# Performance work log

Hardware: AMD Instinct MI355X
Metric: run time of the kernel (lower is better)

## Reference

```python
import jax, jax.numpy as jnp
import numpy as np

T = 2048        # q_len (current chunk)
P = 2048        # past KV cache length
HID = 4096      # hidden_size
H = 32          # num_attention_heads
D = HID // H    # head_dim = 128
THETA = 10000.0


def apply_rope(x, pos):
    # x: [H, T, D], pos: [T] int
    half = D // 2
    inv_freq = 1.0 / (THETA ** (jnp.arange(0, half, dtype=jnp.float32) / half))
    ang = pos.astype(jnp.float32)[:, None] * inv_freq[None, :]      # [T, D/2]
    cos = jnp.concatenate([jnp.cos(ang), jnp.cos(ang)], axis=-1)[None]  # [1, T, D]
    sin = jnp.concatenate([jnp.sin(ang), jnp.sin(ang)], axis=-1)[None]
    rot = jnp.concatenate([-x[..., half:], x[..., :half]], axis=-1)
    return x * cos + rot * sin


def setup_inputs() -> dict:
    key = jax.random.key(0)
    ks = jax.random.split(key, 8)
    s = 1.0 / np.sqrt(HID)
    inp = {
        "hidden_states": jax.random.normal(ks[0], (T, HID), dtype=jnp.float32),
        "attention_mask": jnp.triu(jnp.full((T, T), -jnp.inf, dtype=jnp.float32), k=1),
        "Wq": jax.random.normal(ks[1], (HID, HID), dtype=jnp.float32) * s,
        "Wk": jax.random.normal(ks[2], (HID, HID), dtype=jnp.float32) * s,
        "Wv": jax.random.normal(ks[3], (HID, HID), dtype=jnp.float32) * s,
        "Wo": jax.random.normal(ks[4], (HID, HID), dtype=jnp.float32) * s,
        "past_k": jax.random.normal(ks[5], (H, P, D), dtype=jnp.float32),
        "past_v": jax.random.normal(ks[6], (H, P, D), dtype=jnp.float32),
        "position_ids": P + jnp.arange(T, dtype=jnp.int32),
        "past_length": P,
    }
    return inp


def reference(hidden_states, attention_mask, Wq, Wk, Wv, Wo, past_k, past_v,
              position_ids, past_length):
    # QKV projections -> [H, T, D]
    proj = lambda W: (hidden_states @ W).reshape(T, H, D).transpose(1, 0, 2)
    q, k, v = proj(Wq), proj(Wk), proj(Wv)
    q = apply_rope(q, position_ids)
    k = apply_rope(k, position_ids)

    scale = 1.0 / jnp.sqrt(jnp.float32(D))
    # scores against past cache and current chunk (fp32 softmax, as in source)
    past_dots = (jnp.einsum('htd,hsd->hts', q, past_k) * scale).astype(jnp.float32)
    pmask = jnp.where(jnp.arange(P) < past_length, 0.0, -jnp.inf)  # [P]
    past_dots = past_dots + pmask
    cur = ((jnp.einsum('htd,hsd->hts', q, k) * scale) + attention_mask).astype(jnp.float32)

    # online-softmax merge via logsumexp combination
    past_lse = jax.scipy.special.logsumexp(past_dots, axis=-1, keepdims=True)
    cur_lse = jax.scipy.special.logsumexp(cur, axis=-1, keepdims=True)
    tot_lse = jnp.logaddexp(past_lse, cur_lse)
    pw = jnp.exp(past_dots - tot_lse).astype(q.dtype)
    cw = jnp.exp(cur - tot_lse).astype(q.dtype)

    out = jnp.einsum('hts,hsd->htd', pw, past_v) + jnp.einsum('hts,hsd->htd', cw, v)
    out = jnp.where(past_length == 0,
                    jnp.einsum('hts,hsd->htd', jax.nn.softmax(cur, axis=-1).astype(q.dtype), v),
                    out)
    out = out.transpose(1, 0, 2).reshape(T, HID)   # [T, hidden]
    return out @ Wo
```

## Files before the change

kernel.cpp:

```cpp
#include <hip/hip_runtime.h>
#include <cstdint>
#include <cstddef>

#define T_LEN 2048
#define PAST_MAX 2048
#define HID 4096
#define NHEAD 32
#define DHEAD 128

typedef __bf16 bf16_t;
typedef __bf16 bf16x4 __attribute__((ext_vector_type(4)));
typedef __bf16 bf16x8 __attribute__((ext_vector_type(8)));
typedef float  f32x4  __attribute__((ext_vector_type(4)));
typedef float  f32x16 __attribute__((ext_vector_type(16)));
typedef unsigned int u32x4 __attribute__((ext_vector_type(4)));

__device__ __forceinline__ void gload16(const void* g, void* l){
  __builtin_amdgcn_global_load_lds((const __attribute__((address_space(1))) void*)g,
                                   (__attribute__((address_space(3))) void*)l,
                                   16, 0, 0);
}

__device__ __forceinline__ unsigned pack_bf16(float a, float b){
  const unsigned ua = __builtin_bit_cast(unsigned short, (bf16_t)a);
  const unsigned ub = __builtin_bit_cast(unsigned short, (bf16_t)b);
  return ua | (ub << 16);
}

__global__ void cvt2_k(const float* __restrict__ a, bf16_t* __restrict__ ao,
                       const float* __restrict__ b, bf16_t* __restrict__ bo, int n4){
  int i = blockIdx.x * 256 + threadIdx.x;
  if (i < n4){
    const float4 v = ((const float4*)a)[i];
    bf16x4 o = { (bf16_t)v.x, (bf16_t)v.y, (bf16_t)v.z, (bf16_t)v.w };
    ((bf16x4*)ao)[i] = o;
  } else {
    i -= n4;
    const float4 v = ((const float4*)b)[i];
    bf16x4 o = { (bf16_t)v.x, (bf16_t)v.y, (bf16_t)v.z, (bf16_t)v.w };
    ((bf16x4*)bo)[i] = o;
  }
}

__global__ __launch_bounds__(256) void transpose2_k(const float* __restrict__ in,
                                                    bf16_t* __restrict__ out, int R, int C){
  __shared__ float tile[64][65];
  const int r0 = blockIdx.x << 6, c0 = blockIdx.y << 6;
  const size_t bo = (size_t)blockIdx.z * (size_t)R * (size_t)C;
  const int tx = threadIdx.x & 15, ty = threadIdx.x >> 4;
#pragma unroll
  for (int k = 0; k < 4; ++k){
    const float4 v = *(const float4*)(in + bo + (size_t)(r0 + ty + 16*k) * C + c0 + tx*4);
    float* tp = &tile[ty + 16*k][tx*4];
    tp[0] = v.x; tp[1] = v.y; tp[2] = v.z; tp[3] = v.w;
  }
  __syncthreads();
  const int rr0 = (threadIdx.x & 7) * 8;
  const int ccb = threadIdx.x >> 3;
#pragma unroll
  for (int k = 0; k < 2; ++k){
    const int cc = ccb + 32*k;
    bf16x8 o;
#pragma unroll
    for (int j = 0; j < 8; ++j) o[j] = (bf16_t)tile[rr0 + j][cc];
    *(bf16x8*)(out + bo + (size_t)(c0 + cc) * R + r0 + rr0) = o;
  }
}

__global__ __launch_bounds__(256) void transpose3_k(
    const float* __restrict__ s0, const float* __restrict__ s1, const float* __restrict__ s2,
    bf16_t* __restrict__ d0, bf16_t* __restrict__ d1, bf16_t* __restrict__ d2){
  __shared__ float tile[64][65];
  const float* in = (blockIdx.z == 0) ? s0 : (blockIdx.z == 1) ? s1 : s2;
  bf16_t* out = (blockIdx.z == 0) ? d0 : (blockIdx.z == 1) ? d1 : d2;
  const int r0 = blockIdx.x << 6, c0 = blockIdx.y << 6;
  const int tx = threadIdx.x & 15, ty = threadIdx.x >> 4;
#pragma unroll
  for (int k = 0; k < 4; ++k){
    const float4 v = *(const float4*)(in + (size_t)(r0 + ty + 16*k) * HID + c0 + tx*4);
    float* tp = &tile[ty + 16*k][tx*4];
    tp[0] = v.x; tp[1] = v.y; tp[2] = v.z; tp[3] = v.w;
  }
  __syncthreads();
  const int rr0 = (threadIdx.x & 7) * 8;
  const int ccb = threadIdx.x >> 3;
#pragma unroll
  for (int k = 0; k < 2; ++k){
    const int cc = ccb + 32*k;
    bf16x8 o;
#pragma unroll
    for (int j = 0; j < 8; ++j) o[j] = (bf16_t)tile[rr0 + j][cc];
    *(bf16x8*)(out + (size_t)(c0 + cc) * HID + r0 + rr0) = o;
  }
}

__global__ void ropek_k(bf16_t* __restrict__ K, const int* __restrict__ pos){
  const int idx = blockIdx.x * 256 + threadIdx.x;
  const int i = idx & 63;
  const int t = (idx >> 6) & (T_LEN - 1);
  const int h = idx >> 17;
  const size_t base = ((size_t)h * T_LEN + t) * DHEAD;
  const float p = (float)pos[t];
  const float inv = __expf(-(float)i * 0.14391156605212898f);
  const float ang = p * inv;
  float sn, cs;
  sincosf(ang, &sn, &cs);
  const float b0 = (float)K[base + i], b1 = (float)K[base + i + 64];
  K[base + i]      = (bf16_t)(b0 * cs - b1 * sn);
  K[base + i + 64] = (bf16_t)(b1 * cs + b0 * sn);
}

__global__ __launch_bounds__(512, 1) void gemmqkv4p_k(
    const bf16_t* __restrict__ A,
    const bf16_t* __restrict__ B0, const bf16_t* __restrict__ B1, const bf16_t* __restrict__ B2,
    bf16_t* __restrict__ OQ, bf16_t* __restrict__ OK2, bf16_t* __restrict__ OVT, int cpx)
{
  const int bid = blockIdx.x;
  const int wg  = (bid & 7) * cpx + (bid >> 3);
  const int mt  = wg & 7;
  const int rest = wg >> 3;
  const int z   = rest >> 5;
  const int nt  = rest & 31;
  const int m0  = mt << 8;
  const int n0  = nt << 7;
  const bf16_t* __restrict__ B = (z == 0) ? B0 : (z == 1) ? B1 : B2;

  const int tid = threadIdx.x;
  const int wv = tid >> 6, lane = tid & 63, lm = lane & 15, g = lane >> 4;
  const int wr = wv >> 1, wc = wv & 1;

  __shared__ __align__(16) char smem[98304];

  const f32x4 fzero = {0.f, 0.f, 0.f, 0.f};
  f32x4 acc[4][4];
#pragma unroll
  for (int i = 0; i < 4; ++i)
#pragma unroll
    for (int j = 0; j < 4; ++j) acc[i][j] = fzero;

  int srow[2], schk[2];
#pragma unroll
  for (int i = 0; i < 2; ++i){
    const int c = i * 512 + tid;
    srow[i] = c >> 3;
    schk[i] = (c & 7) ^ (srow[i] & 7);
  }
  const int sdst0 = ((0 * 512 + wv * 64) << 4);
  const int sdst1 = ((1 * 512 + wv * 64) << 4);

  auto stg = [&](int kt, int op){
    if (kt < 64){
      char* dst = smem + (kt & 1) * 49152 + op * 16384;
      const bf16_t* base = (op < 2) ? A + (size_t)(m0 + (op << 7)) * HID
                                    : B + (size_t)n0 * HID;
      base += kt * 64;
      gload16(base + (size_t)srow[0] * HID + schk[0] * 8, dst + sdst0);
      gload16(base + (size_t)srow[1] * HID + schk[1] * 8, dst + sdst1);
    }
  };

  const int koff0 = ((g)     ^ (lm & 7)) << 4;
  const int koff1 = ((4 + g) ^ (lm & 7)) << 4;
  const int abase = ((wr >> 1) << 14) + ((((wr & 1) << 6) + lm) << 7);
  const int bbase = 32768 + ((((wc << 6)) + lm) << 7);

  bf16x8 bfr[4][2];
  auto dsB = [&](int buf){
    const char* p = smem + buf * 49152 + bbase;
#pragma unroll
    for (int ni = 0; ni < 4; ++ni){
      bfr[ni][0] = *(const bf16x8*)(p + ni * 2048 + koff0);
      bfr[ni][1] = *(const bf16x8*)(p + ni * 2048 + koff1);
    }
  };

  stg(0, 2);
  stg(0, 0); stg(0, 1);
  stg(1, 2);
  asm volatile("s_waitcnt vmcnt(2)" ::: "memory");
  __builtin_amdgcn_s_barrier();

  for (int t = 0; t < 32; ++t){
    const int c0 = 2 * t, c1 = 2 * t + 1;
    const bool last = (t == 31);

#pragma unroll
    for (int half = 0; half < 2; ++half){
      const char* bufp = smem + half * 49152;
      bf16x8 afr[2][2];
      dsB(half);
#pragma unroll
      for (int mf = 0; mf < 2; ++mf){
        afr[mf][0] = *(const bf16x8*)(bufp + abase + mf * 2048 + koff0);
        afr[mf][1] = *(const bf16x8*)(bufp + abase + mf * 2048 + koff1);
      }
      if (half == 0){ stg(c1, 0); stg(c1, 1); }
      else          { stg(c0 + 2, 0); stg(c0 + 2, 1); }
      __builtin_amdgcn_s_barrier();
      asm volatile("s_waitcnt lgkmcnt(0)" ::: "memory");
      __builtin_amdgcn_s_setprio(1);
#pragma unroll
      for (int kk = 0; kk < 2; ++kk)
#pragma unroll
        for (int mf = 0; mf < 2; ++mf)
#pragma unroll
          for (int ni = 0; ni < 4; ++ni)
            acc[mf][ni] = __builtin_amdgcn_mfma_f32_16x16x32_bf16(afr[mf][kk], bfr[ni][kk], acc[mf][ni], 0, 0, 0);
      __builtin_amdgcn_s_setprio(0);
      __builtin_amdgcn_s_barrier();

#pragma unroll
      for (int mf = 0; mf < 2; ++mf){
        afr[mf][0] = *(const bf16x8*)(bufp + abase + (mf + 2) * 2048 + koff0);
        afr[mf][1] = *(const bf16x8*)(bufp + abase + (mf + 2) * 2048 + koff1);
      }
      if (half == 0) stg(c0 + 2, 2);
      else           stg(c1 + 2, 2);
      if (last) asm volatile("s_waitcnt vmcnt(0)" ::: "memory");
      else      asm volatile("s_waitcnt vmcnt(2)" ::: "memory");
      __builtin_amdgcn_s_barrier();
      asm volatile("s_waitcnt lgkmcnt(0)" ::: "memory");
      __builtin_amdgcn_s_setprio(1);
#pragma unroll
      for (int kk = 0; kk < 2; ++kk)
#pragma unroll
        for (int mf = 0; mf < 2; ++mf)
#pragma unroll
          for (int ni = 0; ni < 4; ++ni)
            acc[mf + 2][ni] = __builtin_amdgcn_mfma_f32_16x16x32_bf16(afr[mf][kk], bfr[ni][kk], acc[mf + 2][ni], 0, 0, 0);
      __builtin_amdgcn_s_setprio(0);
      __builtin_amdgcn_s_barrier();
    }
  }

#pragma unroll
  for (int ni = 0; ni < 4; ++ni){
    const int col = n0 + wc * 64 + ni * 16 + lm;
    const int hh = col >> 7, dd = col & 127;
#pragma unroll
    for (int mf = 0; mf < 4; ++mf)
#pragma unroll
      for (int r = 0; r < 4; ++r){
        const int trow = m0 + wr * 64 + mf * 16 + g * 4 + r;
        const bf16_t v = (bf16_t)acc[mf][ni][r];
        if (z == 2)      OVT[((size_t)hh * DHEAD + dd) * T_LEN + trow] = v;
        else if (z == 1) OK2[((size_t)hh * T_LEN + trow) * DHEAD + dd] = v;
        else             OQ [((size_t)hh * T_LEN + trow) * DHEAD + dd] = v;
      }
  }
}

__global__ __launch_bounds__(512, 1) void gemm4p_k(
    const bf16_t* __restrict__ A, const bf16_t* __restrict__ B,
    float* __restrict__ OF, int cpx)
{
  const int bid = blockIdx.x;
  const int wg  = (bid & 7) * cpx + (bid >> 3);
  const int mt  = wg & 7;
  const int nt  = wg >> 3;
  const int m0  = mt << 8;
  const int n0  = nt << 7;

  const int tid = threadIdx.x;
  const int wv = tid >> 6, lane = tid & 63, lm = lane & 15, g = lane >> 4;
  const int wr = wv >> 1, wc = wv & 1;

  __shared__ __align__(16) char smem[98304];

  const f32x4 fzero = {0.f, 0.f, 0.f, 0.f};
  f32x4 acc[4][4];
#pragma unroll
  for (int i = 0; i < 4; ++i)
#pragma unroll
    for (int j = 0; j < 4; ++j) acc[i][j] = fzero;

  int srow[2], schk[2];
#pragma unroll
  for (int i = 0; i < 2; ++i){
    const int c = i * 512 + tid;
    srow[i] = c >> 3;
    schk[i] = (c & 7) ^ (srow[i] & 7);
  }
  const int sdst0 = ((0 * 512 + wv * 64) << 4);
  const int sdst1 = ((1 * 512 + wv * 64) << 4);

  auto stg = [&](int kt, int op){
    if (kt < 64){
      char* dst = smem + (kt & 1) * 49152 + op * 16384;
      const bf16_t* base = (op < 2) ? A + (size_t)(m0 + (op << 7)) * HID
                                    : B + (size_t)n0 * HID;
      base += kt * 64;
      gload16(base + (size_t)srow[0] * HID + schk[0] * 8, dst + sdst0);
      gload16(base + (size_t)srow[1] * HID + schk[1] * 8, dst + sdst1);
    }
  };

  const int koff0 = ((g)     ^ (lm & 7)) << 4;
  const int koff1 = ((4 + g) ^ (lm & 7)) << 4;
  const int abase = ((wr >> 1) << 14) + ((((wr & 1) << 6) + lm) << 7);
  const int bbase = 32768 + ((((wc << 6)) + lm) << 7);

  bf16x8 bfr[4][2];
  auto dsB = [&](int buf){
    const char* p = smem + buf * 49152 + bbase;
#pragma unroll
    for (int ni = 0; ni < 4; ++ni){
      bfr[ni][0] = *(const bf16x8*)(p + ni * 2048 + koff0);
      bfr[ni][1] = *(const bf16x8*)(p + ni * 2048 + koff1);
    }
  };

  stg(0, 2);
  stg(0, 0); stg(0, 1);
  stg(1, 2);
  asm volatile("s_waitcnt vmcnt(2)" ::: "memory");
  __builtin_amdgcn_s_barrier();

  for (int t = 0; t < 32; ++t){
    const int c0 = 2 * t, c1 = 2 * t + 1;
    const bool last = (t == 31);

#pragma unroll
    for (int half = 0; half < 2; ++half){
      const char* bufp = smem + half * 49152;
      bf16x8 afr[2][2];
      dsB(half);
#pragma unroll
      for (int mf = 0; mf < 2; ++mf){
        afr[mf][0] = *(const bf16x8*)(bufp + abase + mf * 2048 + koff0);
        afr[mf][1] = *(const bf16x8*)(bufp + abase + mf * 2048 + koff1);
      }
      if (half == 0){ stg(c1, 0); stg(c1, 1); }
      else          { stg(c0 + 2, 0); stg(c0 + 2, 1); }
      __builtin_amdgcn_s_barrier();
      asm volatile("s_waitcnt lgkmcnt(0)" ::: "memory");
      __builtin_amdgcn_s_setprio(1);
#pragma unroll
      for (int kk = 0; kk < 2; ++kk)
#pragma unroll
        for (int mf = 0; mf < 2; ++mf)
#pragma unroll
          for (int ni = 0; ni < 4; ++ni)
            acc[mf][ni] = __builtin_amdgcn_mfma_f32_16x16x32_bf16(afr[mf][kk], bfr[ni][kk], acc[mf][ni], 0, 0, 0);
      __builtin_amdgcn_s_setprio(0);
      __builtin_amdgcn_s_barrier();

#pragma unroll
      for (int mf = 0; mf < 2; ++mf){
        afr[mf][0] = *(const bf16x8*)(bufp + abase + (mf + 2) * 2048 + koff0);
        afr[mf][1] = *(const bf16x8*)(bufp + abase + (mf + 2) * 2048 + koff1);
      }
      if (half == 0) stg(c0 + 2, 2);
      else           stg(c1 + 2, 2);
      if (last) asm volatile("s_waitcnt vmcnt(0)" ::: "memory");
      else      asm volatile("s_waitcnt vmcnt(2)" ::: "memory");
      __builtin_amdgcn_s_barrier();
      asm volatile("s_waitcnt lgkmcnt(0)" ::: "memory");
      __builtin_amdgcn_s_setprio(1);
#pragma unroll
      for (int kk = 0; kk < 2; ++kk)
#pragma unroll
        for (int mf = 0; mf < 2; ++mf)
#pragma unroll
          for (int ni = 0; ni < 4; ++ni)
            acc[mf + 2][ni] = __builtin_amdgcn_mfma_f32_16x16x32_bf16(afr[mf][kk], bfr[ni][kk], acc[mf + 2][ni], 0, 0, 0);
      __builtin_amdgcn_s_setprio(0);
      __builtin_amdgcn_s_barrier();
    }
  }

#pragma unroll
  for (int ni = 0; ni < 4; ++ni){
    const int col = n0 + wc * 64 + ni * 16 + lm;
#pragma unroll
    for (int mf = 0; mf < 4; ++mf)
#pragma unroll
      for (int r = 0; r < 4; ++r){
        const int trow = m0 + wr * 64 + mf * 16 + g * 4 + r;
        OF[(size_t)trow * HID + col] = acc[mf][ni][r];
      }
  }
}

__global__ __launch_bounds__(256, 2) void attn2_k(
    const bf16_t* __restrict__ Q,
    const bf16_t* __restrict__ Kc,
    const bf16_t* __restrict__ VTc,
    const bf16_t* __restrict__ Kp,
    const bf16_t* __restrict__ VTp,
    bf16_t* __restrict__ Ctx,
    const int* __restrict__ plen_p,
    const int* __restrict__ pos)
{
  const int bid = blockIdx.x;
  const int xcd = bid & 7;
  const int k   = bid >> 3;
  const int ho  = k >> 4;
  const int qraw= k & 15;
  const int h   = (xcd << 2) | ho;
  const int qb  = (ho & 2) ? (15 - qraw) : qraw;

  const int tid = threadIdx.x;
  const int w = tid >> 6, lane = tid & 63, l31 = lane & 31, hi = lane >> 5;
  const int qw0 = qb * 128 + w * 32;
  const int qrow = qw0 + l31;
  const int plen = plen_p[0];
  const int npast = (plen + 63) >> 6;
  const int NT = npast + 2 * qb + 2;

  __shared__ __align__(16) char smem[65536 + 512];
  float* lred = (float*)(smem + 65536);

  const bf16_t* qbase = Q + ((size_t)h * T_LEN + qrow) * DHEAD;
  bf16x8 qf[8];
#pragma unroll
  for (int dc = 0; dc < 8; ++dc)
    qf[dc] = *(const bf16x8*)(qbase + dc * 16 + 8 * hi);
  {
    const float ppos = (float)pos[qrow];
    const float qs = 0.08838834764831845f;
#pragma unroll
    for (int dc = 0; dc < 4; ++dc)
#pragma unroll
      for (int j = 0; j < 8; ++j){
        const int fi = dc * 16 + 8 * hi + j;
        const float invf = __expf(-(float)fi * 0.14391156605212898f);
        float sn, cs;
        sincosf(ppos * invf, &sn, &cs);
        const float a0 = (float)qf[dc][j], a1 = (float)qf[dc + 4][j];
        qf[dc][j]     = (bf16_t)((a0 * cs - a1 * sn) * qs);
        qf[dc + 4][j] = (bf16_t)((a1 * cs + a0 * sn) * qs);
      }
  }
  __builtin_amdgcn_sched_barrier(0);

  const f32x16 fz = {0.f,0.f,0.f,0.f,0.f,0.f,0.f,0.f,0.f,0.f,0.f,0.f,0.f,0.f,0.f,0.f};
  f32x16 o[4] = {fz, fz, fz, fz};
  float m = -1e30f, l = 0.f;

  auto stage = [&](int t, int buf){
    const bf16_t* kb; const bf16_t* vb;
    if (t < npast){
      const int s0 = t * 64;
      kb = Kp  + ((size_t)h * PAST_MAX + s0) * DHEAD;
      vb = VTp + (size_t)h * DHEAD * PAST_MAX + s0;
    } else {
      const int s0 = (t - npast) * 64;
      kb = Kc  + ((size_t)h * T_LEN + s0) * DHEAD;
      vb = VTc + (size_t)h * DHEAD * T_LEN + s0;
    }
    char* kl = smem + buf * 32768;
    char* vl = kl + 16384;
#pragma unroll
    for (int i = 0; i < 4; ++i){
      const int c = i * 256 + w * 64 + lane;
      const int krow = c >> 4, kcol = c & 15;
      gload16(kb + (size_t)krow * DHEAD + ((kcol ^ (krow & 7)) << 3), kl + (i * 256 + w * 64) * 16);
      const int vrow = c >> 3, vcol = c & 7;
      gload16(vb + (size_t)vrow * 2048 + ((vcol ^ (vrow & 7)) << 3), vl + (i * 256 + w * 64) * 16);
    }
  };

  stage(0, 0);
  __builtin_amdgcn_sched_barrier(0);

  for (int t = 0; t < NT; ++t){
    const int cur = t & 1;
    if (t + 1 < NT){
      stage(t + 1, cur ^ 1);
      asm volatile("s_waitcnt vmcnt(8)" ::: "memory");
    } else {
      asm volatile("s_waitcnt vmcnt(0)" ::: "memory");
    }
    __builtin_amdgcn_sched_barrier(0);
    __builtin_amdgcn_s_barrier();
    __builtin_amdgcn_sched_barrier(0);

    const bool isc = (t >= npast);
    const int s0c = (t - npast) * 64;
    const bool active = !isc || (s0c <= qw0 + 31);

    if (active){
      char* kl = smem + cur * 32768;
      char* vl = kl + 16384;

      f32x16 sacc[2] = {fz, fz};
      __builtin_amdgcn_s_setprio(1);
#pragma unroll
      for (int kvh = 0; kvh < 2; ++kvh){
        const int krow = (kvh << 5) + l31;
        const int kbo = krow << 8;
        const int sw = (krow & 7) << 4;
#pragma unroll
        for (int dc = 0; dc < 8; ++dc){
          const bf16x8 kf = *(const bf16x8*)(kl + kbo + ((dc * 32 + 16 * hi) ^ sw));
          sacc[kvh] = __builtin_amdgcn_mfma_f32_32x32x16_bf16(kf, qf[dc], sacc[kvh], 0, 0, 0);
        }
      }
      __builtin_amdgcn_s_setprio(0);

      const bool mcur  = isc && (s0c + 63 > qw0);
      const bool mpast = !isc && ((t + 1) * 64 > plen);
      float pv[2][16];
      float pm = -1e30f;
      if (mcur | mpast){
#pragma unroll
        for (int kvh = 0; kvh < 2; ++kvh)
#pragma unroll
          for (int r = 0; r < 16; ++r){
            float x = sacc[kvh][r];
            const int kvoff = (kvh << 5) + (r & 3) + 8 * (r >> 2) + 4 * hi;
            if (mcur  && (s0c + kvoff >  qrow)) x = -1e30f;
            if (mpast && (t * 64 + kvoff >= plen)) x = -1e30f;
            pv[kvh][r] = x;
            pm = fmaxf(pm, x);
          }
      } else {
#pragma unroll
        for (int kvh = 0; kvh < 2; ++kvh)
#pragma unroll
          for (int r = 0; r < 16; ++r){
            pv[kvh][r] = sacc[kvh][r];
            pm = fmaxf(pm, sacc[kvh][r]);
          }
      }
      pm = fmaxf(pm, __shfl_xor(pm, 32));

      if (!__all(pm - m <= 8.f)){
        const float mn = fmaxf(m, pm);
        const float corr = __expf(m - mn);
        m = mn;
        l *= corr;
        if (hi == 0) lred[(w << 5) + l31] = corr;
        asm volatile("s_waitcnt lgkmcnt(0)" ::: "memory");
#pragma unroll
        for (int r = 0; r < 16; ++r){
          const float cc = lred[(w << 5) + (r & 3) + 8 * (r >> 2) + 4 * hi];
#pragma unroll
          for (int nb = 0; nb < 4; ++nb) o[nb][r] *= cc;
        }
      }

      float sum = 0.f;
#pragma unroll
      for (int kvh = 0; kvh < 2; ++kvh)
#pragma unroll
        for (int r = 0; r < 16; ++r){
          const float pe = __expf(pv[kvh][r] - m);
          pv[kvh][r] = pe;
          sum += pe;
        }
      sum += __shfl_xor(sum, 32);
      l += sum;

      unsigned wds[2][8];
#pragma unroll
      for (int kvh = 0; kvh < 2; ++kvh)
#pragma unroll
        for (int i = 0; i < 8; ++i)
          wds[kvh][i] = pack_bf16(pv[kvh][2 * i], pv[kvh][2 * i + 1]);

      bf16x8 pf[4];
#pragma unroll
      for (int ks = 0; ks < 4; ++ks){
        const int s = ks & 1, kvh = ks >> 1;
        const unsigned a0 = hi ? wds[kvh][4 * s]     : wds[kvh][4 * s + 2];
        const unsigned a1 = hi ? wds[kvh][4 * s + 1] : wds[kvh][4 * s + 3];
        const unsigned z0 = (unsigned)__shfl_xor((int)a0, 32);
        const unsigned z1 = (unsigned)__shfl_xor((int)a1, 32);
        u32x4 fw;
        fw[0] = hi ? z0 : wds[kvh][4 * s];
        fw[1] = hi ? z1 : wds[kvh][4 * s + 1];
        fw[2] = hi ? wds[kvh][4 * s + 2] : z0;
        fw[3] = hi ? wds[kvh][4 * s + 3] : z1;
        pf[ks] = __builtin_bit_cast(bf16x8, fw);
      }

      __builtin_amdgcn_s_setprio(1);
#pragma unroll
      for (int ks = 0; ks < 4; ++ks)
#pragma unroll
        for (int nb = 0; nb < 4; ++nb){
          const int vrow = (nb << 5) + l31;
          const bf16x8 vf = *(const bf16x8*)(vl + (vrow << 7) + ((ks * 32 + 16 * hi) ^ ((vrow & 7) << 4)));
          o[nb] = __builtin_amdgcn_mfma_f32_32x32x16_bf16(pf[ks], vf, o[nb], 0, 0, 0);
        }
      __builtin_amdgcn_s_setprio(0);
    }
    __builtin_amdgcn_sched_barrier(0);
    __builtin_amdgcn_s_barrier();
  }

  if (hi == 0) lred[(w << 5) + l31] = l;
  asm volatile("s_waitcnt lgkmcnt(0)" ::: "memory");
#pragma unroll
  for (int r = 0; r < 16; ++r){
    const int cr = (r & 3) + 8 * (r >> 2) + 4 * hi;
    const float li = 1.f / lred[(w << 5) + cr];
    const int trow = qw0 + cr;
    bf16_t* cb = Ctx + (size_t)trow * HID + h * DHEAD + l31;
#pragma unroll
    for (int nb = 0; nb < 4; ++nb)
      cb[nb << 5] = (bf16_t)(o[nb][r] * li);
  }
}

extern "C" void kernel_launch(void* const* d_in, const int* in_sizes, int n_in,
                              void* d_out, int out_size, void* d_ws, size_t ws_size,
                              hipStream_t stream)
{
  const float* X   = (const float*)d_in[0];
  const float* Wq  = (const float*)d_in[2];
  const float* Wk  = (const float*)d_in[3];
  const float* Wv  = (const float*)d_in[4];
  const float* Wo  = (const float*)d_in[5];
  const float* PKi = (const float*)d_in[6];
  const float* PVi = (const float*)d_in[7];
  const int* POS   = (const int*)d_in[8];
  const int* PLEN  = (const int*)d_in[9];
  float* OUT = (float*)d_out;

  char* ws = (char*)d_ws;
  const size_t SZ_XB  = (size_t)T_LEN * HID * 2;
  const size_t SZ_W   = (size_t)HID * HID * 2;
  const size_t SZ_HTD = (size_t)NHEAD * T_LEN * DHEAD * 2;

  bf16_t* XB  = (bf16_t*)(ws);
  bf16_t* WT0 = (bf16_t*)(ws + SZ_XB);
  bf16_t* WT1 = (bf16_t*)(ws + SZ_XB + SZ_W);
  bf16_t* WT2 = (bf16_t*)(ws + SZ_XB + 2 * SZ_W);
  char* p = ws + SZ_XB + 3 * SZ_W;
  bf16_t* QB   = (bf16_t*)p; p += SZ_HTD;
  bf16_t* KB   = (bf16_t*)p; p += SZ_HTD;
  bf16_t* VTB  = (bf16_t*)p; p += SZ_HTD;
  bf16_t* KPB  = (bf16_t*)p; p += SZ_HTD;
  bf16_t* VPTB = (bf16_t*)p; p += SZ_HTD;
  bf16_t* CTX  = (bf16_t*)p; p += SZ_HTD;
  bf16_t* WOT  = QB;

  dim3 blk256(256);
  dim3 blk512(512);
  cvt2_k<<<16384, blk256, 0, stream>>>(X, XB, PKi, KPB, T_LEN * HID / 4);
  transpose3_k<<<dim3(64,64,3), blk256, 0, stream>>>(Wq, Wk, Wv, WT0, WT1, WT2);
  transpose2_k<<<dim3(32,2,32), blk256, 0, stream>>>(PVi, VPTB, PAST_MAX, DHEAD);

  gemmqkv4p_k<<<768, blk512, 0, stream>>>(XB, WT0, WT1, WT2, QB, KB, VTB, 96);
  ropek_k<<<16384, blk256, 0, stream>>>(KB, POS);
  attn2_k<<<512, blk256, 0, stream>>>(QB, KB, VTB, KPB, VPTB, CTX, PLEN, POS);

  transpose2_k<<<dim3(64,64,1), blk256, 0, stream>>>(Wo, WOT, HID, HID);
  gemm4p_k<<<256, blk512, 0, stream>>>(CTX, WOT, OUT, 32);
}
```

Baseline: 582.4 us.

## Enlarge QKV GEMM tile to 256x256 with a new double-buffered pipeline

```diff
diff --git a/kernel.cpp b/kernel.cpp
--- a/kernel.cpp
+++ b/kernel.cpp
@@ -110,7 +110,7 @@
   K[base + i + 64] = (bf16_t)(b1 * cs + b0 * sn);
 }
 
-__global__ __launch_bounds__(512, 1) void gemmqkv4p_k(
+__global__ __launch_bounds__(512, 1) void gemmqkv256_k(
     const bf16_t* __restrict__ A,
     const bf16_t* __restrict__ B0, const bf16_t* __restrict__ B1, const bf16_t* __restrict__ B2,
     bf16_t* __restrict__ OQ, bf16_t* __restrict__ OK2, bf16_t* __restrict__ OVT, int cpx)
@@ -118,23 +118,22 @@
   const int bid = blockIdx.x;
   const int wg  = (bid & 7) * cpx + (bid >> 3);
   const int mt  = wg & 7;
-  const int rest = wg >> 3;
-  const int z   = rest >> 5;
-  const int nt  = rest & 31;
+  const int nt  = wg >> 3;
+  const int z   = nt >> 4;
   const int m0  = mt << 8;
-  const int n0  = nt << 7;
+  const int n0  = (nt & 15) << 8;
   const bf16_t* __restrict__ B = (z == 0) ? B0 : (z == 1) ? B1 : B2;
 
   const int tid = threadIdx.x;
   const int wv = tid >> 6, lane = tid & 63, lm = lane & 15, g = lane >> 4;
-  const int wr = wv >> 1, wc = wv & 1;
-
-  __shared__ __align__(16) char smem[98304];
+  const int wr = wv >> 2, wc = wv & 3;
+
+  __shared__ __align__(16) char smem[131072];
 
   const f32x4 fzero = {0.f, 0.f, 0.f, 0.f};
-  f32x4 acc[4][4];
-#pragma unroll
-  for (int i = 0; i < 4; ++i)
+  f32x4 acc[8][4];
+#pragma unroll
+  for (int i = 0; i < 8; ++i)
 #pragma unroll
     for (int j = 0; j < 4; ++j) acc[i][j] = fzero;
 
@@ -150,9 +149,9 @@
 
   auto stg = [&](int kt, int op){
     if (kt < 64){
-      char* dst = smem + (kt & 1) * 49152 + op * 16384;
+      char* dst = smem + (kt & 1) * 65536 + op * 16384;
       const bf16_t* base = (op < 2) ? A + (size_t)(m0 + (op << 7)) * HID
-                                    : B + (size_t)n0 * HID;
+                                    : B + (size_t)(n0 + ((op - 2) << 7)) * HID;
       base += kt * 64;
       gload16(base + (size_t)srow[0] * HID + schk[0] * 8, dst + sdst0);
       gload16(base + (size_t)srow[1] * HID + schk[1] * 8, dst + sdst1);
@@ -161,76 +160,61 @@
 
   const int koff0 = ((g)     ^ (lm & 7)) << 4;
   const int koff1 = ((4 + g) ^ (lm & 7)) << 4;
-  const int abase = ((wr >> 1) << 14) + ((((wr & 1) << 6) + lm) << 7);
-  const int bbase = 32768 + ((((wc << 6)) + lm) << 7);
-
-  bf16x8 bfr[4][2];
-  auto dsB = [&](int buf){
-    const char* p = smem + buf * 49152 + bbase;
+  const int abase = (wr << 14) + (lm << 7);
+  const int bbase = ((2 + (wc >> 1)) << 14) + ((((wc & 1) << 6) + lm) << 7);
+
+  stg(0, 0); stg(0, 1); stg(0, 2); stg(0, 3);
+  stg(1, 0); stg(1, 1);
+  asm volatile("s_waitcnt vmcnt(4)" ::: "memory");
+  __builtin_amdgcn_s_barrier();
+
+  for (int t = 0; t < 64; ++t){
+    const char* bufp = smem + (t & 1) * 65536;
+
+    bf16x8 bfr[4][2], afr[4][2];
 #pragma unroll
     for (int ni = 0; ni < 4; ++ni){
-      bfr[ni][0] = *(const bf16x8*)(p + ni * 2048 + koff0);
-      bfr[ni][1] = *(const bf16x8*)(p + ni * 2048 + koff1);
-    }
-  };
-
-  stg(0, 2);
-  stg(0, 0); stg(0, 1);
-  stg(1, 2);
-  asm volatile("s_waitcnt vmcnt(2)" ::: "memory");
-  __builtin_amdgcn_s_barrier();
-
-  for (int t = 0; t < 32; ++t){
-    const int c0 = 2 * t, c1 = 2 * t + 1;
-    const bool last = (t == 31);
-
-#pragma unroll
-    for (int half = 0; half < 2; ++half){
-      const char* bufp = smem + half * 49152;
-      bf16x8 afr[2][2];
-      dsB(half);
-#pragma unroll
-      for (int mf = 0; mf < 2; ++mf){
-        afr[mf][0] = *(const bf16x8*)(bufp + abase + mf * 2048 + koff0);
-        afr[mf][1] = *(const bf16x8*)(bufp + abase + mf * 2048 + koff1);
-      }
-      if (half == 0){ stg(c1, 0); stg(c1, 1); }
-      else          { stg(c0 + 2, 0); stg(c0 + 2, 1); }
-      __builtin_amdgcn_s_barrier();
-      asm volatile("s_waitcnt lgkmcnt(0)" ::: "memory");
-      __builtin_amdgcn_s_setprio(1);
-#pragma unroll
-      for (int kk = 0; kk < 2; ++kk)
-#pragma unroll
-        for (int mf = 0; mf < 2; ++mf)
-#pragma unroll
-          for (int ni = 0; ni < 4; ++ni)
-            acc[mf][ni] = __builtin_amdgcn_mfma_f32_16x16x32_bf16(afr[mf][kk], bfr[ni][kk], acc[mf][ni], 0, 0, 0);
-      __builtin_amdgcn_s_setprio(0);
-      __builtin_amdgcn_s_barrier();
-
-#pragma unroll
-      for (int mf = 0; mf < 2; ++mf){
-        afr[mf][0] = *(const bf16x8*)(bufp + abase + (mf + 2) * 2048 + koff0);
-        afr[mf][1] = *(const bf16x8*)(bufp + abase + (mf + 2) * 2048 + koff1);
-      }
-      if (half == 0) stg(c0 + 2, 2);
-      else           stg(c1 + 2, 2);
-      if (last) asm volatile("s_waitcnt vmcnt(0)" ::: "memory");
-      else      asm volatile("s_waitcnt vmcnt(2)" ::: "memory");
-      __builtin_amdgcn_s_barrier();
-      asm volatile("s_waitcnt lgkmcnt(0)" ::: "memory");
-      __builtin_amdgcn_s_setprio(1);
-#pragma unroll
-      for (int kk = 0; kk < 2; ++kk)
-#pragma unroll
-        for (int mf = 0; mf < 2; ++mf)
-#pragma unroll
-          for (int ni = 0; ni < 4; ++ni)
-            acc[mf + 2][ni] = __builtin_amdgcn_mfma_f32_16x16x32_bf16(afr[mf][kk], bfr[ni][kk], acc[mf + 2][ni], 0, 0, 0);
-      __builtin_amdgcn_s_setprio(0);
-      __builtin_amdgcn_s_barrier();
-    }
+      bfr[ni][0] = *(const bf16x8*)(bufp + bbase + ni * 2048 + koff0);
+      bfr[ni][1] = *(const bf16x8*)(bufp + bbase + ni * 2048 + koff1);
+    }
+#pragma unroll
+    for (int mf = 0; mf < 4; ++mf){
+      afr[mf][0] = *(const bf16x8*)(bufp + abase + mf * 2048 + koff0);
+      afr[mf][1] = *(const bf16x8*)(bufp + abase + mf * 2048 + koff1);
+    }
+    stg(t + 1, 2); stg(t + 1, 3);
+    __builtin_amdgcn_s_barrier();
+    asm volatile("s_waitcnt lgkmcnt(0)" ::: "memory");
+    __builtin_amdgcn_s_setprio(1);
+#pragma unroll
+    for (int kk = 0; kk < 2; ++kk)
+#pragma unroll
+      for (int mf = 0; mf < 4; ++mf)
+#pragma unroll
+        for (int ni = 0; ni < 4; ++ni)
+          acc[mf][ni] = __builtin_amdgcn_mfma_f32_16x16x32_bf16(afr[mf][kk], bfr[ni][kk], acc[mf][ni], 0, 0, 0);
+    __builtin_amdgcn_s_setprio(0);
+
+#pragma unroll
+    for (int mf = 0; mf < 4; ++mf){
+      afr[mf][0] = *(const bf16x8*)(bufp + abase + (mf + 4) * 2048 + koff0);
+      afr[mf][1] = *(const bf16x8*)(bufp + abase + (mf + 4) * 2048 + koff1);
+    }
+    asm volatile("s_waitcnt lgkmcnt(0)" ::: "memory");
+    __builtin_amdgcn_s_barrier();
+    stg(t + 2, 0); stg(t + 2, 1);
+    if (t + 2 < 64) asm volatile("s_waitcnt vmcnt(4)" ::: "memory");
+    else            asm volatile("s_waitcnt vmcnt(0)" ::: "memory");
+    __builtin_amdgcn_s_setprio(1);
+#pragma unroll
+    for (int kk = 0; kk < 2; ++kk)
+#pragma unroll
+      for (int mf = 0; mf < 4; ++mf)
+#pragma unroll
+        for (int ni = 0; ni < 4; ++ni)
+          acc[mf + 4][ni] = __builtin_amdgcn_mfma_f32_16x16x32_bf16(afr[mf][kk], bfr[ni][kk], acc[mf + 4][ni], 0, 0, 0);
+    __builtin_amdgcn_s_setprio(0);
+    __builtin_amdgcn_s_barrier();
   }
 
 #pragma unroll
@@ -238,10 +222,10 @@
     const int col = n0 + wc * 64 + ni * 16 + lm;
     const int hh = col >> 7, dd = col & 127;
 #pragma unroll
-    for (int mf = 0; mf < 4; ++mf)
+    for (int mf = 0; mf < 8; ++mf)
 #pragma unroll
       for (int r = 0; r < 4; ++r){
-        const int trow = m0 + wr * 64 + mf * 16 + g * 4 + r;
+        const int trow = m0 + wr * 128 + mf * 16 + g * 4 + r;
         const bf16_t v = (bf16_t)acc[mf][ni][r];
         if (z == 2)      OVT[((size_t)hh * DHEAD + dd) * T_LEN + trow] = v;
         else if (z == 1) OK2[((size_t)hh * T_LEN + trow) * DHEAD + dd] = v;
@@ -644,7 +628,7 @@
   transpose3_k<<<dim3(64,64,3), blk256, 0, stream>>>(Wq, Wk, Wv, WT0, WT1, WT2);
   transpose2_k<<<dim3(32,2,32), blk256, 0, stream>>>(PVi, VPTB, PAST_MAX, DHEAD);
 
-  gemmqkv4p_k<<<768, blk512, 0, stream>>>(XB, WT0, WT1, WT2, QB, KB, VTB, 96);
+  gemmqkv256_k<<<384, blk512, 0, stream>>>(XB, WT0, WT1, WT2, QB, KB, VTB, 48);
   ropek_k<<<16384, blk256, 0, stream>>>(KB, POS);
   attn2_k<<<512, blk256, 0, stream>>>(QB, KB, VTB, KPB, VPTB, CTX, PLEN, POS);
 
```

Result: slower. 602.0 us (+3.4%).
